# Performance work log

Measured on AMD Instinct MI355X. Metric: run time of the kernel, lower is better.

The kernel has to match this reference:

```python
import jax, jax.numpy as jnp
import numpy as np

N = 600            # total detections across TTA views
H = 384
W = 384
NUM_CLASSES = 9
SIGMA = 0.5            # soft-NMS gaussian sigma (source default)
SCORE_THRESH = 0.001   # soft-NMS survival threshold (source default)
MASK_IOU_THRESH = 0.5  # _average_overlapping_masks threshold


def box_iou(a, b):
    # a: [N,4], b: [M,4] in xyxy -> [N,M] IoU (matches torchvision.ops.box_iou)
    area_a = (a[:, 2] - a[:, 0]) * (a[:, 3] - a[:, 1])
    area_b = (b[:, 2] - b[:, 0]) * (b[:, 3] - b[:, 1])
    lt = jnp.maximum(a[:, None, :2], b[None, :, :2])
    rb = jnp.minimum(a[:, None, 2:], b[None, :, 2:])
    wh = jnp.clip(rb - lt, 0.0)
    inter = wh[..., 0] * wh[..., 1]
    return inter / (area_a[:, None] + area_b[None, :] - inter)


def soft_nms(shifted_boxes, scores):
    """Sequential gaussian soft-NMS. Returns (keep_mask, decayed_scores) in
    ORIGINAL index order. Processes detections in descending-score order;
    each kept detection decays later scores by exp(-iou^2/sigma); detections
    whose decayed score drops <= SCORE_THRESH are removed."""
    order = jnp.argsort(-scores)
    b = shifted_boxes[order]
    s0 = scores[order]
    ious = box_iou(b, b)  # [N,N], precomputed rows reused in the scan
    idx = jnp.arange(N)

    def body(i, carry):
        s, active, keep = carry
        is_act = active[i]
        decay = jnp.exp(-(ious[i] ** 2) / SIGMA)  # [N]
        app = (idx > i) & is_act
        s2 = jnp.where(app, s * decay, s)
        active2 = active & jnp.where(app, s2 > SCORE_THRESH, True)
        keep2 = keep.at[i].set(is_act)
        return (s2, active2, keep2)

    s_f, _, keep_sorted = jax.lax.fori_loop(
        0, N, body, (s0, jnp.ones((N,), bool), jnp.zeros((N,), bool)))
    keep = jnp.zeros((N,), bool).at[order].set(keep_sorted)
    dec = jnp.zeros((N,), s_f.dtype).at[order].set(s_f)
    return keep, dec


def setup_inputs() -> dict:
    key = jax.random.key(0)
    k1, k2, k3, k4, k5 = jax.random.split(key, 5)
    # valid xyxy boxes inside a WxH image
    x1 = jax.random.uniform(k1, (N,), minval=0.0, maxval=W - 130.0)
    y1 = jax.random.uniform(k2, (N,), minval=0.0, maxval=H - 130.0)
    wh = jax.random.uniform(k3, (N, 2), minval=8.0, maxval=128.0)
    boxes = jnp.stack([x1, y1, x1 + wh[:, 0], y1 + wh[:, 1]], axis=1).astype(jnp.float32)
    scores = jax.random.uniform(k4, (N,), dtype=jnp.float32)
    labels = jax.random.randint(k5, (N,), 0, NUM_CLASSES, dtype=jnp.int32)
    masks = jax.random.uniform(jax.random.fold_in(key, 7), (N, 1, H, W), dtype=jnp.float32)
    return {"boxes": boxes, "scores": scores, "masks": masks, "labels": labels}


def reference(boxes, scores, masks, labels):
    # --- class-aware shift so NMS never crosses classes ---
    max_coord = boxes.max() + 1.0
    shifted = boxes + (labels.astype(boxes.dtype) * max_coord)[:, None]
    # --- soft-NMS ---
    keep, dec_scores = soft_nms(shifted, scores)
    kept_scores = jnp.where(keep, dec_scores, 0.0)
    # --- cross-view mask averaging over same-class, high-IoU matches ---
    ious = box_iou(boxes, boxes)  # unshifted boxes, as in source
    match = (labels[:, None] == labels[None, :]) & (ious > MASK_IOU_THRESH)  # [N,N]
    cnt = match.sum(axis=1)  # includes self-match for every row
    mf = match.astype(masks.dtype)
    flat = masks.reshape(N, -1)                      # [N, H*W]
    avg = (mf @ flat) / jnp.maximum(cnt, 1).astype(masks.dtype)[:, None]
    use_avg = keep & (cnt > 1)
    out_masks = jnp.where(use_avg[:, None], avg, flat).reshape(masks.shape)
    return keep, kept_scores, out_masks
```

## Files before the change

kernel.cpp:

```cpp
#include <hip/hip_runtime.h>

#define NDET 600
#define IMG_HW (384 * 384)
#define NF4 (IMG_HW / 4)
#define NMS_BLK 640
#define SCORE_THRESH 0.001f

__global__ __launch_bounds__(NMS_BLK) void nms_kernel(
    const float* __restrict__ boxes, const float* __restrict__ scores,
    const int* __restrict__ labels, float* __restrict__ out_keep,
    float* __restrict__ out_score, int* __restrict__ keep_ws)
{
    const int tid = threadIdx.x;

    __shared__ float s_sc[NDET];
    __shared__ float sx1[NDET], sy1[NDET], sx2[NDET], sy2[NDET];
    __shared__ float bx1[NDET], by1[NDET], bx2[NDET], by2[NDET];
    __shared__ float bar[NDET], bsc[NDET];
    __shared__ int   borig[NDET];
    __shared__ int   sact[NDET];
    __shared__ float sred[NMS_BLK];

    if (tid < NDET) s_sc[tid] = scores[tid];

    float m = -1e30f;
    for (int k = tid; k < NDET * 4; k += NMS_BLK) m = fmaxf(m, boxes[k]);
    sred[tid] = m;
    __syncthreads();
    for (int off = NMS_BLK / 2; off > 0; off >>= 1) {
        if (tid < off) sred[tid] = fmaxf(sred[tid], sred[tid + off]);
        __syncthreads();
    }
    const float max_coord = sred[0] + 1.0f;

    if (tid < NDET) {
        const float shf = (float)labels[tid] * max_coord;
        sx1[tid] = boxes[4 * tid + 0] + shf;
        sy1[tid] = boxes[4 * tid + 1] + shf;
        sx2[tid] = boxes[4 * tid + 2] + shf;
        sy2[tid] = boxes[4 * tid + 3] + shf;
        sact[tid] = 1;
    }
    __syncthreads();

    if (tid < NDET) {
        const float s_i = s_sc[tid];
        int r = 0;
        for (int j = 0; j < NDET; j++) {
            const float s_j = s_sc[j];
            r += (s_j > s_i) || (s_j == s_i && j < tid);
        }
        bx1[r] = sx1[tid]; by1[r] = sy1[tid];
        bx2[r] = sx2[tid]; by2[r] = sy2[tid];
        bar[r] = (sx2[tid] - sx1[tid]) * (sy2[tid] - sy1[tid]);
        bsc[r] = s_i;
        borig[r] = tid;
    }
    __syncthreads();

    float myx1 = 0.f, myy1 = 0.f, myx2 = 0.f, myy2 = 0.f, mya = 0.f, mys = 0.f;
    int myact = 0, myorig = 0;
    if (tid < NDET) {
        myx1 = bx1[tid]; myy1 = by1[tid]; myx2 = bx2[tid]; myy2 = by2[tid];
        mya = bar[tid];  mys = bsc[tid];  myorig = borig[tid];
        myact = 1;
    }
    __syncthreads();

    for (int i = 0; i < NDET; i++) {
        const int act_i = sact[i];
        if (act_i) {
            const float ix1 = bx1[i], iy1 = by1[i], ix2 = bx2[i], iy2 = by2[i];
            const float ia = bar[i];
            if (tid > i && tid < NDET && myact) {
                const float w = fminf(myx2, ix2) - fmaxf(myx1, ix1);
                const float h = fminf(myy2, iy2) - fmaxf(myy1, iy1);
                if (w > 0.f && h > 0.f) {
                    const float inter = w * h;
                    const float iou = inter / (mya + ia - inter);
                    mys *= expf(-(iou * iou) / 0.5f);
                    if (!(mys > SCORE_THRESH)) { myact = 0; sact[tid] = 0; }
                }
            }
        }
        __syncthreads();
    }

    if (tid < NDET) {
        out_keep[myorig]  = myact ? 1.0f : 0.0f;
        out_score[myorig] = myact ? mys : 0.0f;
        keep_ws[myorig]   = myact;
    }
}

__global__ __launch_bounds__(256) void match_kernel(
    const float* __restrict__ boxes, const int* __restrict__ labels,
    const int* __restrict__ keep_ws, int* __restrict__ cnt_ws,
    int* __restrict__ ua_ws, int* __restrict__ list_ws)
{
    const int i = blockIdx.x;
    const int tid = threadIdx.x;
    __shared__ int mflag[NDET];

    const float ix1 = boxes[4 * i + 0], iy1 = boxes[4 * i + 1];
    const float ix2 = boxes[4 * i + 2], iy2 = boxes[4 * i + 3];
    const float ia = (ix2 - ix1) * (iy2 - iy1);
    const int li = labels[i];

    for (int j = tid; j < NDET; j += 256) {
        const float jx1 = boxes[4 * j + 0], jy1 = boxes[4 * j + 1];
        const float jx2 = boxes[4 * j + 2], jy2 = boxes[4 * j + 3];
        const float ja = (jx2 - jx1) * (jy2 - jy1);
        float w = fminf(ix2, jx2) - fmaxf(ix1, jx1);
        float h = fminf(iy2, jy2) - fmaxf(iy1, jy1);
        w = fmaxf(w, 0.f); h = fmaxf(h, 0.f);
        const float inter = w * h;
        const float iou = inter / (ia + ja - inter);
        mflag[j] = (labels[j] == li) && (iou > 0.5f);
    }
    __syncthreads();

    if (tid == 0) {
        int c = 0;
        for (int j = 0; j < NDET; j++)
            if (mflag[j]) list_ws[i * NDET + (c++)] = j;
        cnt_ws[i] = c;
        ua_ws[i] = (keep_ws[i] && c > 1) ? 1 : 0;
    }
}

__global__ __launch_bounds__(256) void mask_kernel(
    const float4* __restrict__ masks, const int* __restrict__ cnt_ws,
    const int* __restrict__ ua_ws, const int* __restrict__ list_ws,
    float4* __restrict__ out)
{
    const int row = blockIdx.y;
    const int c4 = blockIdx.x * 256 + threadIdx.x;

    float4 r;
    if (!ua_ws[row]) {
        r = masks[(size_t)row * NF4 + c4];
    } else {
        const int c = cnt_ws[row];
        float4 acc = make_float4(0.f, 0.f, 0.f, 0.f);
        for (int k = 0; k < c; k++) {
            const int j = list_ws[row * NDET + k];
            const float4 v = masks[(size_t)j * NF4 + c4];
            acc.x += v.x; acc.y += v.y; acc.z += v.z; acc.w += v.w;
        }
        const float fc = (float)c;
        r.x = acc.x / fc; r.y = acc.y / fc; r.z = acc.z / fc; r.w = acc.w / fc;
    }
    out[(size_t)row * NF4 + c4] = r;
}

extern "C" void kernel_launch(void* const* d_in, const int* in_sizes, int n_in,
                              void* d_out, int out_size, void* d_ws, size_t ws_size,
                              hipStream_t stream) {
    const float* boxes  = (const float*)d_in[0];
    const float* scores = (const float*)d_in[1];
    const float* masks  = (const float*)d_in[2];
    const int*   labels = (const int*)d_in[3];

    float* out = (float*)d_out;

    int* keep_ws = (int*)d_ws;
    int* cnt_ws  = keep_ws + NDET;
    int* ua_ws   = cnt_ws + NDET;
    int* list_ws = ua_ws + NDET;

    nms_kernel<<<1, NMS_BLK, 0, stream>>>(boxes, scores, labels,
                                          out, out + NDET, keep_ws);
    match_kernel<<<NDET, 256, 0, stream>>>(boxes, labels, keep_ws,
                                           cnt_ws, ua_ws, list_ws);
    mask_kernel<<<dim3(NF4 / 256, NDET), 256, 0, stream>>>(
        (const float4*)masks, cnt_ws, ua_ws, list_ws,
        (float4*)(out + 2 * NDET));
}
```

Baseline: 802.1 us.

## Run soft-NMS in a single wavefront with register slots and shuffles

Restructures the sequential soft-NMS kernel from a 640-thread block with a block barrier per detection to one 64-lane wavefront holding ten detections per lane in registers. Broadcasting the current box uses wave shuffles, so the per-iteration __syncthreads and shared-memory active flags go away. The max reduction and rank sort are also done per wave with more work per lane. The cost is more serial work per lane and higher register pressure.

```diff
diff --git a/kernel.cpp b/kernel.cpp
--- a/kernel.cpp
+++ b/kernel.cpp
@@ -3,93 +3,124 @@
 #define NDET 600
 #define IMG_HW (384 * 384)
 #define NF4 (IMG_HW / 4)
-#define NMS_BLK 640
+#define SLOTS 10
 #define SCORE_THRESH 0.001f
 
-__global__ __launch_bounds__(NMS_BLK) void nms_kernel(
-    const float* __restrict__ boxes, const float* __restrict__ scores,
+__global__ __launch_bounds__(64) void nms_kernel(
+    const float4* __restrict__ boxes4, const float* __restrict__ scores,
     const int* __restrict__ labels, float* __restrict__ out_keep,
     float* __restrict__ out_score, int* __restrict__ keep_ws)
 {
-    const int tid = threadIdx.x;
+    const int l = threadIdx.x;
 
     __shared__ float s_sc[NDET];
-    __shared__ float sx1[NDET], sy1[NDET], sx2[NDET], sy2[NDET];
-    __shared__ float bx1[NDET], by1[NDET], bx2[NDET], by2[NDET];
-    __shared__ float bar[NDET], bsc[NDET];
-    __shared__ int   borig[NDET];
-    __shared__ int   sact[NDET];
-    __shared__ float sred[NMS_BLK];
-
-    if (tid < NDET) s_sc[tid] = scores[tid];
+    __shared__ float wx1[NDET], wy1[NDET], wx2[NDET], wy2[NDET];
+    __shared__ float war[NDET], wsc[NDET];
+    __shared__ int   worig[NDET];
+
+    for (int t = l; t < NDET; t += 64) s_sc[t] = scores[t];
 
     float m = -1e30f;
-    for (int k = tid; k < NDET * 4; k += NMS_BLK) m = fmaxf(m, boxes[k]);
-    sred[tid] = m;
+    for (int t = l; t < NDET; t += 64) {
+        const float4 b = boxes4[t];
+        m = fmaxf(fmaxf(m, fmaxf(b.x, b.y)), fmaxf(b.z, b.w));
+    }
+    #pragma unroll
+    for (int off = 32; off; off >>= 1) m = fmaxf(m, __shfl_xor(m, off));
+    const float max_coord = m + 1.0f;
+
     __syncthreads();
-    for (int off = NMS_BLK / 2; off > 0; off >>= 1) {
-        if (tid < off) sred[tid] = fmaxf(sred[tid], sred[tid + off]);
-        __syncthreads();
-    }
-    const float max_coord = sred[0] + 1.0f;
-
-    if (tid < NDET) {
-        const float shf = (float)labels[tid] * max_coord;
-        sx1[tid] = boxes[4 * tid + 0] + shf;
-        sy1[tid] = boxes[4 * tid + 1] + shf;
-        sx2[tid] = boxes[4 * tid + 2] + shf;
-        sy2[tid] = boxes[4 * tid + 3] + shf;
-        sact[tid] = 1;
+
+    float ox1[SLOTS], oy1[SLOTS], ox2[SLOTS], oy2[SLOTS], osc[SLOTS];
+    int   rank[SLOTS];
+    #pragma unroll
+    for (int k = 0; k < SLOTS; ++k) {
+        const int t = l + 64 * k;
+        if (t < NDET) {
+            const float4 b = boxes4[t];
+            const float shf = (float)labels[t] * max_coord;
+            ox1[k] = b.x + shf; oy1[k] = b.y + shf;
+            ox2[k] = b.z + shf; oy2[k] = b.w + shf;
+            osc[k] = s_sc[t];
+            rank[k] = 0;
+        }
+    }
+    for (int j = 0; j < NDET; ++j) {
+        const float sj = s_sc[j];
+        #pragma unroll
+        for (int k = 0; k < SLOTS; ++k) {
+            const int t = l + 64 * k;
+            if (t < NDET)
+                rank[k] += (sj > osc[k]) || (sj == osc[k] && j < t);
+        }
+    }
+    #pragma unroll
+    for (int k = 0; k < SLOTS; ++k) {
+        const int t = l + 64 * k;
+        if (t < NDET) {
+            const int r = rank[k];
+            wx1[r] = ox1[k]; wy1[r] = oy1[k];
+            wx2[r] = ox2[k]; wy2[r] = oy2[k];
+            war[r] = (ox2[k] - ox1[k]) * (oy2[k] - oy1[k]);
+            wsc[r] = osc[k];
+            worig[r] = t;
+        }
     }
     __syncthreads();
 
-    if (tid < NDET) {
-        const float s_i = s_sc[tid];
-        int r = 0;
-        for (int j = 0; j < NDET; j++) {
-            const float s_j = s_sc[j];
-            r += (s_j > s_i) || (s_j == s_i && j < tid);
-        }
-        bx1[r] = sx1[tid]; by1[r] = sy1[tid];
-        bx2[r] = sx2[tid]; by2[r] = sy2[tid];
-        bar[r] = (sx2[tid] - sx1[tid]) * (sy2[tid] - sy1[tid]);
-        bsc[r] = s_i;
-        borig[r] = tid;
-    }
-    __syncthreads();
-
-    float myx1 = 0.f, myy1 = 0.f, myx2 = 0.f, myy2 = 0.f, mya = 0.f, mys = 0.f;
-    int myact = 0, myorig = 0;
-    if (tid < NDET) {
-        myx1 = bx1[tid]; myy1 = by1[tid]; myx2 = bx2[tid]; myy2 = by2[tid];
-        mya = bar[tid];  mys = bsc[tid];  myorig = borig[tid];
-        myact = 1;
-    }
-    __syncthreads();
-
-    for (int i = 0; i < NDET; i++) {
-        const int act_i = sact[i];
-        if (act_i) {
-            const float ix1 = bx1[i], iy1 = by1[i], ix2 = bx2[i], iy2 = by2[i];
-            const float ia = bar[i];
-            if (tid > i && tid < NDET && myact) {
-                const float w = fminf(myx2, ix2) - fmaxf(myx1, ix1);
-                const float h = fminf(myy2, iy2) - fmaxf(myy1, iy1);
-                if (w > 0.f && h > 0.f) {
-                    const float inter = w * h;
-                    const float iou = inter / (mya + ia - inter);
-                    mys *= expf(-(iou * iou) / 0.5f);
-                    if (!(mys > SCORE_THRESH)) { myact = 0; sact[tid] = 0; }
+    float rx1[SLOTS], ry1[SLOTS], rx2[SLOTS], ry2[SLOTS], ra[SLOTS], rs[SLOTS];
+    int   rorig[SLOTS];
+    int   actmask = 0;
+    #pragma unroll
+    for (int k = 0; k < SLOTS; ++k) {
+        const int p = l + 64 * k;
+        if (p < NDET) {
+            rx1[k] = wx1[p]; ry1[k] = wy1[p];
+            rx2[k] = wx2[p]; ry2[k] = wy2[p];
+            ra[k]  = war[p]; rs[k]  = wsc[p];
+            rorig[k] = worig[p];
+            actmask |= 1 << k;
+        }
+    }
+
+    #pragma unroll
+    for (int s = 0; s < SLOTS; ++s) {
+        const int base = s * 64;
+        const int nIn = (NDET - base) < 64 ? (NDET - base) : 64;
+        for (int li = 0; li < nIn; ++li) {
+            const int am = __shfl(actmask, li);
+            if (!((am >> s) & 1)) continue;
+            const float ix1 = __shfl(rx1[s], li);
+            const float iy1 = __shfl(ry1[s], li);
+            const float ix2 = __shfl(rx2[s], li);
+            const float iy2 = __shfl(ry2[s], li);
+            const float ia  = __shfl(ra[s],  li);
+            #pragma unroll
+            for (int k = s; k < SLOTS; ++k) {
+                const bool applies = (k > s) || (l > li);
+                if (applies && ((actmask >> k) & 1)) {
+                    const float w = fminf(rx2[k], ix2) - fmaxf(rx1[k], ix1);
+                    const float h = fminf(ry2[k], iy2) - fmaxf(ry1[k], iy1);
+                    if (w > 0.f && h > 0.f) {
+                        const float inter = w * h;
+                        const float iou = inter / (ra[k] + ia - inter);
+                        rs[k] *= expf(-(iou * iou) / 0.5f);
+                        if (!(rs[k] > SCORE_THRESH)) actmask &= ~(1 << k);
+                    }
                 }
             }
         }
-        __syncthreads();
-    }
-
-    if (tid < NDET) {
-        out_keep[myorig]  = myact ? 1.0f : 0.0f;
-        out_score[myorig] = myact ? mys : 0.0f;
-        keep_ws[myorig]   = myact;
+    }
+
+    #pragma unroll
+    for (int k = 0; k < SLOTS; ++k) {
+        const int p = l + 64 * k;
+        if (p < NDET) {
+            const int a = (actmask >> k) & 1;
+            out_keep[rorig[k]]  = a ? 1.0f : 0.0f;
+            out_score[rorig[k]] = a ? rs[k] : 0.0f;
+            keep_ws[rorig[k]]   = a;
+        }
     }
 }
 
@@ -169,8 +200,8 @@
     int* ua_ws   = cnt_ws + NDET;
     int* list_ws = ua_ws + NDET;
 
-    nms_kernel<<<1, NMS_BLK, 0, stream>>>(boxes, scores, labels,
-                                          out, out + NDET, keep_ws);
+    nms_kernel<<<1, 64, 0, stream>>>((const float4*)boxes, scores, labels,
+                                     out, out + NDET, keep_ws);
     match_kernel<<<NDET, 256, 0, stream>>>(boxes, labels, keep_ws,
                                            cnt_ws, ua_ws, list_ws);
     mask_kernel<<<dim3(NF4 / 256, NDET), 256, 0, stream>>>(
```

Result: slower. 1.231 ms (+53.5%).
